# Performance work log

Measured on AMD Instinct MI355X. Metric: run time of the kernel, lower is better.

The kernel has to match this reference:

```python
import jax, jax.numpy as jnp
import numpy as np

N, K, D = 65536, 1024, 256


def setup_inputs() -> dict:
    key = jax.random.key(0)
    k1, k2 = jax.random.split(key)
    input_data = jax.random.normal(k1, (N, D), dtype=jnp.float32)
    codebooks = jax.random.normal(k2, (K, D), dtype=jnp.float32)
    return {"input_data": input_data, "codebooks": codebooks}


def reference(input_data, codebooks):
    # Squared Euclidean distances [N, K] via the expanded form
    # in the torch source, without the [N, D, K] intermediate).
    x_sq = jnp.sum(input_data * input_data, axis=-1, keepdims=True)      # [N, 1]
    c_sq = jnp.sum(codebooks * codebooks, axis=-1)                       # [K]
    distances = x_sq + c_sq[None, :] - 2.0 * (input_data @ codebooks.T)  # [N, K]

    min_indices = jnp.argmin(distances, axis=1)                          # [N]
    quantized_input = codebooks[min_indices]                             # [N, D]

    loss = jnp.mean(jnp.square(input_data - quantized_input))

    # avg_probs = mean over rows of one_hot(min_indices, K) == counts / N
    counts = jnp.zeros((K,), dtype=jnp.float32).at[min_indices].add(1.0)
    avg_probs = counts / jnp.float32(N)
    perplexity = jnp.exp(-jnp.sum(avg_probs * jnp.log(avg_probs + 1e-10)))

    return quantized_input, loss, perplexity, min_indices
```

## Files before the change

### kernel.cpp

```cpp
#include <hip/hip_runtime.h>
#include <math.h>

#define N_ROWS 65536
#define K_CODES 1024
#define D_DIM 256
#define TAU 0.12f

#define WS_NFLAG   0
#define WS_CSQ     16
#define WS_COUNTS  4112
#define WS_MINIDX  8208
#define WS_LIST    270352
#define WS_PART    532496
#define WS_CSQD    536592
#define WS_CBH     544784

typedef _Float16 f16x8 __attribute__((ext_vector_type(8)));
typedef float    f32x4 __attribute__((ext_vector_type(4)));

__device__ __forceinline__ void gl_lds16(const _Float16* g, _Float16* l) {
    __builtin_amdgcn_global_load_lds(
        (const __attribute__((address_space(1))) unsigned int*)g,
        (__attribute__((address_space(3))) unsigned int*)l, 16, 0, 0);
}

__global__ __launch_bounds__(256) void k_prep(
    const float* __restrict__ cb, _Float16* __restrict__ cbh,
    float* __restrict__ csq, double* __restrict__ csqd,
    float* __restrict__ cbT, unsigned* __restrict__ counts,
    unsigned* __restrict__ nflag)
{
    const int b2 = blockIdx.x;
    const int t = threadIdx.x;
    const long idx8 = (long)b2 * 2048 + t * 8;
    float4 v0 = *(const float4*)(cb + idx8);
    float4 v1 = *(const float4*)(cb + idx8 + 4);
    f16x8 h;
    h[0] = (_Float16)v0.x; h[1] = (_Float16)v0.y; h[2] = (_Float16)v0.z; h[3] = (_Float16)v0.w;
    h[4] = (_Float16)v1.x; h[5] = (_Float16)v1.y; h[6] = (_Float16)v1.z; h[7] = (_Float16)v1.w;
    *(f16x8*)(cbh + idx8) = h;
    {
        const int row = b2 * 8 + (t >> 5);
        const int col = (t & 31) * 8;
        cbT[(col + 0) * 1024 + row] = v0.x;
        cbT[(col + 1) * 1024 + row] = v0.y;
        cbT[(col + 2) * 1024 + row] = v0.z;
        cbT[(col + 3) * 1024 + row] = v0.w;
        cbT[(col + 4) * 1024 + row] = v1.x;
        cbT[(col + 5) * 1024 + row] = v1.y;
        cbT[(col + 6) * 1024 + row] = v1.z;
        cbT[(col + 7) * 1024 + row] = v1.w;
    }
    double sqd = (double)v0.x * v0.x + (double)v0.y * v0.y
               + (double)v0.z * v0.z + (double)v0.w * v0.w
               + (double)v1.x * v1.x + (double)v1.y * v1.y
               + (double)v1.z * v1.z + (double)v1.w * v1.w;
    for (int off = 16; off > 0; off >>= 1) sqd += __shfl_down(sqd, off, 32);
    if ((t & 31) == 0) {
        csqd[b2 * 8 + (t >> 5)] = sqd;
        csq[b2 * 8 + (t >> 5)] = (float)sqd;
    }
    if (b2 < 4) counts[b2 * 256 + t] = 0u;
    if (b2 == 0 && t == 0) *nflag = 0u;
}

__device__ __forceinline__ void merge2(float& m1, int& i1, float& m2,
                                       float om1, int oi1, float om2) {
    float hi  = fmaxf(m1, om1);
    float lo2 = fminf(m2, om2);
    bool take = (om1 < m1) || (om1 == m1 && oi1 < i1);
    if (take) { m1 = om1; i1 = oi1; }
    m2 = fminf(hi, lo2);
}

__global__ __launch_bounds__(256, 2) void k_main(
    const float* __restrict__ x, const _Float16* __restrict__ cbh,
    const float* __restrict__ csq,
    int* __restrict__ min_idx, int* __restrict__ list,
    unsigned* __restrict__ nflag, double* __restrict__ partials)
{
    __shared__ __attribute__((aligned(16))) _Float16 Bs[2][128 * 64];
    __shared__ float  xsq_s[128];
    __shared__ double wred[4];

    const int tid  = threadIdx.x;
    const int w    = tid >> 6;
    const int lane = tid & 63;
    const int rlow = lane & 15;
    const int quad = lane >> 4;
    const long n0  = (long)blockIdx.x * 128;

#pragma unroll
    for (int r = 0; r < 4; ++r) {
        int o = r * 256 + tid;
        int row = o >> 3, s = o & 7, g = s ^ (row & 7);
        gl_lds16(cbh + (long)row * 256 + g * 8, Bs[0] + o * 8);
    }

    f16x8 a_reg[8][2];
#pragma unroll
    for (int i = 0; i < 2; ++i) {
        float cs[8];
        const float* rp = x + (n0 + w * 32 + i * 16 + rlow) * 256;
#pragma unroll
        for (int c = 0; c < 8; ++c) {
            const float* src = rp + c * 32 + quad * 8;
            float4 v0 = *(const float4*)src;
            float4 v1 = *(const float4*)(src + 4);
            f16x8 h;
            h[0] = (_Float16)v0.x; h[1] = (_Float16)v0.y; h[2] = (_Float16)v0.z; h[3] = (_Float16)v0.w;
            h[4] = (_Float16)v1.x; h[5] = (_Float16)v1.y; h[6] = (_Float16)v1.z; h[7] = (_Float16)v1.w;
            a_reg[c][i] = h;
            cs[c] = v0.x * v0.x + v0.y * v0.y + v0.z * v0.z + v0.w * v0.w
                  + v1.x * v1.x + v1.y * v1.y + v1.z * v1.z + v1.w * v1.w;
        }
        float s1_0 = cs[0] + cs[4], s1_1 = cs[1] + cs[5];
        float s1_2 = cs[2] + cs[6], s1_3 = cs[3] + cs[7];
        float s2_0 = s1_0 + s1_2, s2_1 = s1_1 + s1_3;
        float s3 = s2_0 + s2_1;
        float s4 = s3 + __shfl_down(s3, 32, 64);
        float s5 = s4 + __shfl_down(s4, 16, 64);
        if (quad == 0) xsq_s[w * 32 + i * 16 + rlow] = s5;
    }

    float sm1[8], sm2[8];
    int   si1[8];
#pragma unroll
    for (int s = 0; s < 8; s++) { sm1[s] = INFINITY; sm2[s] = INFINITY; si1[s] = 0; }

    f32x4 acc[16];
    const f32x4 z = {0.f, 0.f, 0.f, 0.f};
#pragma unroll
    for (int t2 = 0; t2 < 16; t2++) acc[t2] = z;

    __syncthreads();

    for (int p = 0; p < 32; ++p) {
        const int cur = p & 1;
        if (p < 31) {
            const int pn = p + 1;
            const long kb = (long)(pn >> 2) * 128;
            const int d0 = (pn & 3) * 64;
            _Float16* dst = Bs[cur ^ 1];
#pragma unroll
            for (int r = 0; r < 4; ++r) {
                int o = r * 256 + tid;
                int row = o >> 3, s = o & 7, g = s ^ (row & 7);
                gl_lds16(cbh + (kb + row) * 256 + d0 + g * 8, dst + o * 8);
            }
        }
        const int kt = p >> 2, dblk = p & 3;
        const _Float16* B = Bs[cur];
#pragma unroll
        for (int h = 0; h < 2; ++h) {
            f16x8 b[8];
#pragma unroll
            for (int j = 0; j < 8; ++j) {
                int row = j * 16 + rlow;
                int s = (h * 4 + quad) ^ (rlow & 7);
                b[j] = *(const f16x8*)&B[row * 64 + s * 8];
            }
            const int c = dblk * 2 + h;
#pragma unroll
            for (int i = 0; i < 2; ++i)
#pragma unroll
                for (int j = 0; j < 8; ++j)
                    acc[i * 8 + j] = __builtin_amdgcn_mfma_f32_16x16x32_f16(
                        a_reg[c][i], b[j], acc[i * 8 + j], 0, 0, 0);
        }
        if (dblk == 3) {
            const int kbase = kt * 128;
#pragma unroll
            for (int j = 0; j < 8; ++j) {
                const int code = kbase + j * 16 + rlow;
                const float csj = csq[code];
#pragma unroll
                for (int i = 0; i < 2; ++i)
#pragma unroll
                    for (int v = 0; v < 4; ++v) {
                        const int s = i * 4 + v;
                        float val = fmaf(-2.f, acc[i * 8 + j][v], csj);
                        bool lt = val < sm1[s];
                        sm2[s] = fminf(fmaxf(val, sm1[s]), sm2[s]);
                        si1[s] = lt ? code : si1[s];
                        sm1[s] = fminf(val, sm1[s]);
                    }
            }
#pragma unroll
            for (int t2 = 0; t2 < 16; ++t2) acc[t2] = z;
        }
        __syncthreads();
    }

#pragma unroll
    for (int s = 0; s < 8; ++s) {
#pragma unroll
        for (int m = 1; m < 16; m <<= 1) {
            float om1 = __shfl_xor(sm1[s], m, 64);
            float om2 = __shfl_xor(sm2[s], m, 64);
            int   oi1 = __shfl_xor(si1[s], m, 64);
            merge2(sm1[s], si1[s], sm2[s], om1, oi1, om2);
        }
    }

    double lsum = 0.0;
    if (rlow == 0) {
#pragma unroll
        for (int i = 0; i < 2; ++i)
#pragma unroll
            for (int v = 0; v < 4; ++v) {
                const int s = i * 4 + v;
                const int rl = w * 32 + i * 16 + quad * 4 + v;
                const long n = n0 + rl;
                min_idx[n] = si1[s];
                if (sm2[s] - sm1[s] < TAU) {
                    unsigned pp = atomicAdd(nflag, 1u);
                    list[pp] = (int)n;
                }
                lsum += (double)xsq_s[rl] + (double)sm1[s];
            }
    }
    lsum += __shfl_down(lsum, 32, 64);
    lsum += __shfl_down(lsum, 16, 64);
    if (lane == 0) wred[w] = lsum;
    __syncthreads();
    if (tid == 0) partials[blockIdx.x] = ((wred[0] + wred[1]) + wred[2]) + wred[3];
}

#define RPB 2
__global__ __launch_bounds__(256) void k_refine(
    const float* __restrict__ x, const float* __restrict__ cbT,
    const double* __restrict__ csqd, const unsigned* __restrict__ nflag,
    const int* __restrict__ list, int* __restrict__ min_idx)
{
    __shared__ double xsd[RPB][256];
    __shared__ double rbv[RPB][4];
    __shared__ int    rbi[RPB][4];
    const int tid = threadIdx.x;
    const int w = tid >> 6, lane = tid & 63;
    const unsigned nf = *nflag;
    const int k0 = tid * 4;

    for (unsigned base = blockIdx.x * RPB; base < nf; base += gridDim.x * RPB) {
        __syncthreads();
#pragma unroll
        for (int r = 0; r < RPB; ++r) {
            unsigned it = base + r; if (it > nf - 1) it = nf - 1;
            int ridx = list[it];
            xsd[r][tid] = (double)x[(long)ridx * D_DIM + tid];
        }
        __syncthreads();

        double s0[RPB], s1[RPB], s2[RPB], s3[RPB];
#pragma unroll
        for (int r = 0; r < RPB; ++r) { s0[r] = 0.0; s1[r] = 0.0; s2[r] = 0.0; s3[r] = 0.0; }

#pragma unroll 4
        for (int d = 0; d < D_DIM; ++d) {
            float4 c = *(const float4*)(cbT + d * 1024 + k0);
            double c0 = (double)c.x, c1 = (double)c.y;
            double c2 = (double)c.z, c3 = (double)c.w;
#pragma unroll
            for (int r = 0; r < RPB; ++r) {
                double xv = xsd[r][d];
                s0[r] = fma(xv, c0, s0[r]);
                s1[r] = fma(xv, c1, s1[r]);
                s2[r] = fma(xv, c2, s2[r]);
                s3[r] = fma(xv, c3, s3[r]);
            }
        }

        double best[RPB]; int bidx[RPB];
#pragma unroll
        for (int r = 0; r < RPB; ++r) { best[r] = 1e300; bidx[r] = 0; }
        {
            const double ck0 = csqd[k0];
            const double ck1 = csqd[k0 + 1];
            const double ck2 = csqd[k0 + 2];
            const double ck3 = csqd[k0 + 3];
#pragma unroll
            for (int r = 0; r < RPB; ++r) {
                double dd;
                dd = fma(-2.0, s0[r], ck0);
                if (dd < best[r] || (dd == best[r] && k0 < bidx[r])) { best[r] = dd; bidx[r] = k0; }
                dd = fma(-2.0, s1[r], ck1);
                if (dd < best[r] || (dd == best[r] && k0 + 1 < bidx[r])) { best[r] = dd; bidx[r] = k0 + 1; }
                dd = fma(-2.0, s2[r], ck2);
                if (dd < best[r] || (dd == best[r] && k0 + 2 < bidx[r])) { best[r] = dd; bidx[r] = k0 + 2; }
                dd = fma(-2.0, s3[r], ck3);
                if (dd < best[r] || (dd == best[r] && k0 + 3 < bidx[r])) { best[r] = dd; bidx[r] = k0 + 3; }
            }
        }

#pragma unroll
        for (int r = 0; r < RPB; ++r) {
            double bv = best[r]; int bi = bidx[r];
            for (int off = 32; off > 0; off >>= 1) {
                double od = __shfl_down(bv, off, 64);
                int    oi = __shfl_down(bi, off, 64);
                if (od < bv || (od == bv && oi < bi)) { bv = od; bi = oi; }
            }
            if (lane == 0) { rbv[r][w] = bv; rbi[r][w] = bi; }
        }
        __syncthreads();
        if (tid < RPB && base + tid < nf) {
            double bb = rbv[tid][0]; int bi_ = rbi[tid][0];
#pragma unroll
            for (int wv = 1; wv < 4; ++wv) {
                if (rbv[tid][wv] < bb || (rbv[tid][wv] == bb && rbi[tid][wv] < bi_)) {
                    bb = rbv[tid][wv]; bi_ = rbi[tid][wv];
                }
            }
            min_idx[list[base + tid]] = bi_;
        }
    }
}

__global__ __launch_bounds__(256) void k_out(
    const float* __restrict__ cb, const int* __restrict__ min_idx,
    float* __restrict__ out, unsigned* __restrict__ counts)
{
    const int tid  = threadIdx.x;
    const int wave = tid >> 6;
    const int lane = tid & 63;
    const long n = (long)blockIdx.x * 4 + wave;
    const int idx = min_idx[n];

    float4 q = *(const float4*)(cb + (long)idx * D_DIM + lane * 4);
    *(float4*)(out + n * D_DIM + lane * 4) = q;

    if (lane == 0) {
        atomicAdd(&counts[idx], 1u);
        out[16777218L + n] = (float)idx;
    }
}

__global__ void k_final(const double* __restrict__ partials,
                        const unsigned* __restrict__ counts, float* __restrict__ out)
{
    __shared__ double red[256];
    const int tid = threadIdx.x;

    red[tid] = partials[tid] + partials[tid + 256];
    __syncthreads();
    for (int off = 128; off > 0; off >>= 1) { if (tid < off) red[tid] += red[tid + off]; __syncthreads(); }
    double loss = red[0] / (double)((long)N_ROWS * D_DIM);
    __syncthreads();

    double h = 0.0;
    for (int k = tid; k < K_CODES; k += 256) {
        double p = (double)counts[k] / (double)N_ROWS;
        h += p * log(p + 1e-10);
    }
    red[tid] = h;
    __syncthreads();
    for (int off = 128; off > 0; off >>= 1) { if (tid < off) red[tid] += red[tid + off]; __syncthreads(); }

    if (tid == 0) {
        out[16777216] = (float)loss;
        out[16777217] = (float)exp(-red[0]);
    }
}

extern "C" void kernel_launch(void* const* d_in, const int* in_sizes, int n_in,
                              void* d_out, int out_size, void* d_ws, size_t ws_size,
                              hipStream_t stream)
{
    const float* x  = (const float*)d_in[0];
    const float* cb = (const float*)d_in[1];
    float* out = (float*)d_out;
    char*  ws  = (char*)d_ws;

    unsigned*  nflag    = (unsigned*)(ws + WS_NFLAG);
    float*     csq      = (float*)(ws + WS_CSQ);
    unsigned*  counts   = (unsigned*)(ws + WS_COUNTS);
    int*       min_idx  = (int*)(ws + WS_MINIDX);
    int*       list     = (int*)(ws + WS_LIST);
    double*    partials = (double*)(ws + WS_PART);
    double*    csqd     = (double*)(ws + WS_CSQD);
    _Float16*  cbh      = (_Float16*)(ws + WS_CBH);
    float*     cbT      = out + 8781824L;

    hipLaunchKernelGGL(k_prep,   dim3(128),  dim3(256), 0, stream,
                       cb, cbh, csq, csqd, cbT, counts, nflag);
    hipLaunchKernelGGL(k_main,   dim3(512),  dim3(256), 0, stream,
                       x, cbh, csq, min_idx, list, nflag, partials);
    hipLaunchKernelGGL(k_refine, dim3(1024), dim3(256), 0, stream,
                       x, cbT, csqd, nflag, list, min_idx);
    hipLaunchKernelGGL(k_out,    dim3(N_ROWS / 4), dim3(256), 0, stream,
                       cb, min_idx, out, counts);
    hipLaunchKernelGGL(k_final,  dim3(1), dim3(256), 0, stream, partials, counts, out);
}
```

Baseline: 262.9 us.

## Restructure VQ main kernel: 256-row blocks, 4-stage codebook pipeline, overlapped top-2

Each k_main block now covers 256 rows with 256 blocks, which matches the CU count. The codebook is staged in full-depth 32-code tiles through a 4-buffer LDS ring, and raw vmcnt waits plus barriers are used instead of __syncthreads. The MFMA for one tile runs alongside the top-2 selection of the previous tile through ping-pong accumulators, and codebook norms are cached in LDS. The intent is to double A-register reuse and hide load latency behind compute. In exchange there is only one block per CU, higher register pressure, and a more fragile hand-written schedule. Refine rows per block is raised to 4 and the final reduction is adjusted to the 256 partials.

```diff
diff --git a/kernel.cpp b/kernel.cpp
--- a/kernel.cpp
+++ b/kernel.cpp
@@ -73,14 +73,15 @@
     m2 = fminf(hi, lo2);
 }
 
-__global__ __launch_bounds__(256, 2) void k_main(
+__global__ __launch_bounds__(256, 1) void k_main(
     const float* __restrict__ x, const _Float16* __restrict__ cbh,
     const float* __restrict__ csq,
     int* __restrict__ min_idx, int* __restrict__ list,
     unsigned* __restrict__ nflag, double* __restrict__ partials)
 {
-    __shared__ __attribute__((aligned(16))) _Float16 Bs[2][128 * 64];
-    __shared__ float  xsq_s[128];
+    __shared__ __attribute__((aligned(16))) _Float16 Bs[4][32 * 256];
+    __shared__ __attribute__((aligned(16))) float csq_s[1024];
+    __shared__ float  xsq_s[256];
     __shared__ double wred[4];
 
     const int tid  = threadIdx.x;
@@ -88,20 +89,85 @@
     const int lane = tid & 63;
     const int rlow = lane & 15;
     const int quad = lane >> 4;
-    const long n0  = (long)blockIdx.x * 128;
-
-#pragma unroll
-    for (int r = 0; r < 4; ++r) {
-        int o = r * 256 + tid;
-        int row = o >> 3, s = o & 7, g = s ^ (row & 7);
-        gl_lds16(cbh + (long)row * 256 + g * 8, Bs[0] + o * 8);
-    }
-
-    f16x8 a_reg[8][2];
-#pragma unroll
-    for (int i = 0; i < 2; ++i) {
+    const long n0  = (long)blockIdx.x * 256;
+    const int qxr  = (quad * 16) ^ ((rlow & 7) << 4);
+
+#define STAGE_TILE(T)                                                         \
+    {                                                                         \
+        _Float16* dst_ = Bs[(T) & 3];                                         \
+        _Pragma("unroll")                                                     \
+        for (int r_ = 0; r_ < 4; ++r_) {                                      \
+            int g_ = r_ * 256 + tid;                                          \
+            int row_ = g_ >> 5;                                               \
+            int src_ = ((g_ & 31) << 4) ^ ((row_ & 7) << 4);                  \
+            gl_lds16(cbh + ((long)(T) * 32 + row_) * 256 + (src_ >> 1),       \
+                     dst_ + g_ * 8);                                          \
+        }                                                                     \
+    }
+
+#define WAITB8  { asm volatile("s_waitcnt vmcnt(8)" ::: "memory");            \
+                  __builtin_amdgcn_s_barrier();                               \
+                  __builtin_amdgcn_sched_barrier(0); }
+#define WAITB4  { asm volatile("s_waitcnt vmcnt(4)" ::: "memory");            \
+                  __builtin_amdgcn_s_barrier();                               \
+                  __builtin_amdgcn_sched_barrier(0); }
+#define WAITB0  { asm volatile("s_waitcnt vmcnt(0)" ::: "memory");            \
+                  __builtin_amdgcn_s_barrier();                               \
+                  __builtin_amdgcn_sched_barrier(0); }
+
+#define MFMA_TILE(T, ACC)                                                     \
+    {                                                                         \
+        const char* Bb_ = (const char*)Bs[(T) & 3];                           \
+        _Pragma("unroll")                                                     \
+        for (int kc_ = 0; kc_ < 8; ++kc_) {                                   \
+            f16x8 b0_ = *(const f16x8*)(Bb_ + rlow * 512 + ((kc_ * 64) ^ qxr));        \
+            f16x8 b1_ = *(const f16x8*)(Bb_ + (16 + rlow) * 512 + ((kc_ * 64) ^ qxr)); \
+            _Pragma("unroll")                                                 \
+            for (int i_ = 0; i_ < 4; ++i_) {                                  \
+                if (kc_ == 0) {                                               \
+                    ACC[i_][0] = __builtin_amdgcn_mfma_f32_16x16x32_f16(      \
+                        a_reg[0][i_], b0_, zf4, 0, 0, 0);                     \
+                    ACC[i_][1] = __builtin_amdgcn_mfma_f32_16x16x32_f16(      \
+                        a_reg[0][i_], b1_, zf4, 0, 0, 0);                     \
+                } else {                                                      \
+                    ACC[i_][0] = __builtin_amdgcn_mfma_f32_16x16x32_f16(      \
+                        a_reg[kc_][i_], b0_, ACC[i_][0], 0, 0, 0);            \
+                    ACC[i_][1] = __builtin_amdgcn_mfma_f32_16x16x32_f16(      \
+                        a_reg[kc_][i_], b1_, ACC[i_][1], 0, 0, 0);            \
+                }                                                             \
+            }                                                                 \
+        }                                                                     \
+    }
+
+#define TOP2_TILE(T, ACC)                                                     \
+    {                                                                         \
+        _Pragma("unroll")                                                     \
+        for (int j_ = 0; j_ < 2; ++j_) {                                      \
+            const int code_ = (T) * 32 + j_ * 16 + rlow;                      \
+            const float csj_ = csq_s[code_];                                  \
+            _Pragma("unroll")                                                 \
+            for (int i_ = 0; i_ < 4; ++i_)                                    \
+                _Pragma("unroll")                                             \
+                for (int v_ = 0; v_ < 4; ++v_) {                              \
+                    const int s_ = i_ * 4 + v_;                               \
+                    float val_ = fmaf(-2.f, ACC[i_][j_][v_], csj_);           \
+                    bool lt_ = val_ < sm1[s_];                                \
+                    sm2[s_] = fminf(fmaxf(val_, sm1[s_]), sm2[s_]);           \
+                    si1[s_] = lt_ ? code_ : si1[s_];                          \
+                    sm1[s_] = fminf(val_, sm1[s_]);                           \
+                }                                                             \
+        }                                                                     \
+    }
+
+    STAGE_TILE(0);
+    STAGE_TILE(1);
+    *(float4*)&csq_s[tid * 4] = *(const float4*)&csq[tid * 4];
+
+    f16x8 a_reg[8][4];
+#pragma unroll
+    for (int i = 0; i < 4; ++i) {
         float cs[8];
-        const float* rp = x + (n0 + w * 32 + i * 16 + rlow) * 256;
+        const float* rp = x + (n0 + w * 64 + i * 16 + rlow) * 256;
 #pragma unroll
         for (int c = 0; c < 8; ++c) {
             const float* src = rp + c * 32 + quad * 8;
@@ -120,80 +186,48 @@
         float s3 = s2_0 + s2_1;
         float s4 = s3 + __shfl_down(s3, 32, 64);
         float s5 = s4 + __shfl_down(s4, 16, 64);
-        if (quad == 0) xsq_s[w * 32 + i * 16 + rlow] = s5;
-    }
-
-    float sm1[8], sm2[8];
-    int   si1[8];
-#pragma unroll
-    for (int s = 0; s < 8; s++) { sm1[s] = INFINITY; sm2[s] = INFINITY; si1[s] = 0; }
-
-    f32x4 acc[16];
-    const f32x4 z = {0.f, 0.f, 0.f, 0.f};
-#pragma unroll
-    for (int t2 = 0; t2 < 16; t2++) acc[t2] = z;
+        if (quad == 0) xsq_s[w * 64 + i * 16 + rlow] = s5;
+    }
+
+    float sm1[16], sm2[16];
+    int   si1[16];
+#pragma unroll
+    for (int s = 0; s < 16; s++) { sm1[s] = INFINITY; sm2[s] = INFINITY; si1[s] = 0; }
+
+    f32x4 accA[4][2], accB[4][2];
+    const f32x4 zf4 = {0.f, 0.f, 0.f, 0.f};
 
     __syncthreads();
 
-    for (int p = 0; p < 32; ++p) {
-        const int cur = p & 1;
-        if (p < 31) {
-            const int pn = p + 1;
-            const long kb = (long)(pn >> 2) * 128;
-            const int d0 = (pn & 3) * 64;
-            _Float16* dst = Bs[cur ^ 1];
-#pragma unroll
-            for (int r = 0; r < 4; ++r) {
-                int o = r * 256 + tid;
-                int row = o >> 3, s = o & 7, g = s ^ (row & 7);
-                gl_lds16(cbh + (kb + row) * 256 + d0 + g * 8, dst + o * 8);
-            }
-        }
-        const int kt = p >> 2, dblk = p & 3;
-        const _Float16* B = Bs[cur];
-#pragma unroll
-        for (int h = 0; h < 2; ++h) {
-            f16x8 b[8];
-#pragma unroll
-            for (int j = 0; j < 8; ++j) {
-                int row = j * 16 + rlow;
-                int s = (h * 4 + quad) ^ (rlow & 7);
-                b[j] = *(const f16x8*)&B[row * 64 + s * 8];
-            }
-            const int c = dblk * 2 + h;
-#pragma unroll
-            for (int i = 0; i < 2; ++i)
-#pragma unroll
-                for (int j = 0; j < 8; ++j)
-                    acc[i * 8 + j] = __builtin_amdgcn_mfma_f32_16x16x32_f16(
-                        a_reg[c][i], b[j], acc[i * 8 + j], 0, 0, 0);
-        }
-        if (dblk == 3) {
-            const int kbase = kt * 128;
-#pragma unroll
-            for (int j = 0; j < 8; ++j) {
-                const int code = kbase + j * 16 + rlow;
-                const float csj = csq[code];
-#pragma unroll
-                for (int i = 0; i < 2; ++i)
-#pragma unroll
-                    for (int v = 0; v < 4; ++v) {
-                        const int s = i * 4 + v;
-                        float val = fmaf(-2.f, acc[i * 8 + j][v], csj);
-                        bool lt = val < sm1[s];
-                        sm2[s] = fminf(fmaxf(val, sm1[s]), sm2[s]);
-                        si1[s] = lt ? code : si1[s];
-                        sm1[s] = fminf(val, sm1[s]);
-                    }
-            }
-#pragma unroll
-            for (int t2 = 0; t2 < 16; ++t2) acc[t2] = z;
-        }
-        __syncthreads();
-    }
-
-#pragma unroll
-    for (int s = 0; s < 8; ++s) {
+    STAGE_TILE(2);
+    WAITB8;
+    MFMA_TILE(0, accA);
+
+    for (int tt = 0; tt < 14; ++tt) {
+        const int t1 = 2 * tt + 1, t2 = 2 * tt + 2;
+        STAGE_TILE(t1 + 2);
+        WAITB8;
+        MFMA_TILE(t1, accB);
+        TOP2_TILE(t1 - 1, accA);
+        STAGE_TILE(t2 + 2);
+        WAITB8;
+        MFMA_TILE(t2, accA);
+        TOP2_TILE(t2 - 1, accB);
+    }
+    STAGE_TILE(31);
+    WAITB8;
+    MFMA_TILE(29, accB);
+    TOP2_TILE(28, accA);
+    WAITB4;
+    MFMA_TILE(30, accA);
+    TOP2_TILE(29, accB);
+    WAITB0;
+    MFMA_TILE(31, accB);
+    TOP2_TILE(30, accA);
+    TOP2_TILE(31, accB);
+
+#pragma unroll
+    for (int s = 0; s < 16; ++s) {
 #pragma unroll
         for (int m = 1; m < 16; m <<= 1) {
             float om1 = __shfl_xor(sm1[s], m, 64);
@@ -206,11 +240,11 @@
     double lsum = 0.0;
     if (rlow == 0) {
 #pragma unroll
-        for (int i = 0; i < 2; ++i)
+        for (int i = 0; i < 4; ++i)
 #pragma unroll
             for (int v = 0; v < 4; ++v) {
                 const int s = i * 4 + v;
-                const int rl = w * 32 + i * 16 + quad * 4 + v;
+                const int rl = w * 64 + i * 16 + quad * 4 + v;
                 const long n = n0 + rl;
                 min_idx[n] = si1[s];
                 if (sm2[s] - sm1[s] < TAU) {
@@ -225,9 +259,16 @@
     if (lane == 0) wred[w] = lsum;
     __syncthreads();
     if (tid == 0) partials[blockIdx.x] = ((wred[0] + wred[1]) + wred[2]) + wred[3];
-}
-
-#define RPB 2
+
+#undef STAGE_TILE
+#undef WAITB8
+#undef WAITB4
+#undef WAITB0
+#undef MFMA_TILE
+#undef TOP2_TILE
+}
+
+#define RPB 4
 __global__ __launch_bounds__(256) void k_refine(
     const float* __restrict__ x, const float* __restrict__ cbT,
     const double* __restrict__ csqd, const unsigned* __restrict__ nflag,
@@ -255,7 +296,7 @@
 #pragma unroll
         for (int r = 0; r < RPB; ++r) { s0[r] = 0.0; s1[r] = 0.0; s2[r] = 0.0; s3[r] = 0.0; }
 
-#pragma unroll 4
+#pragma unroll 2
         for (int d = 0; d < D_DIM; ++d) {
             float4 c = *(const float4*)(cbT + d * 1024 + k0);
             double c0 = (double)c.x, c1 = (double)c.y;
@@ -341,7 +382,7 @@
     __shared__ double red[256];
     const int tid = threadIdx.x;
 
-    red[tid] = partials[tid] + partials[tid + 256];
+    red[tid] = partials[tid];
     __syncthreads();
     for (int off = 128; off > 0; off >>= 1) { if (tid < off) red[tid] += red[tid + off]; __syncthreads(); }
     double loss = red[0] / (double)((long)N_ROWS * D_DIM);
@@ -383,7 +424,7 @@
 
     hipLaunchKernelGGL(k_prep,   dim3(128),  dim3(256), 0, stream,
                        cb, cbh, csq, csqd, cbT, counts, nflag);
-    hipLaunchKernelGGL(k_main,   dim3(512),  dim3(256), 0, stream,
+    hipLaunchKernelGGL(k_main,   dim3(256),  dim3(256), 0, stream,
                        x, cbh, csq, min_idx, list, nflag, partials);
     hipLaunchKernelGGL(k_refine, dim3(1024), dim3(256), 0, stream,
                        x, cbT, csqd, nflag, list, min_idx);
```

After: 252.3 us. -4.0%, faster.
